# Optimization experiments

Measured on AMD Instinct MI355X. Metric: run time of the kernel, lower is better.

The kernel has to match this reference:

```python
import jax, jax.numpy as jnp
import numpy as np

B, T, HID = 2, 1024, 2048
NH, NKV, HD = 16, 4, 128
L, INTER = 4, 5632
EPS = 1e-6


def _rope_tables(key):
    inv_freq = 1.0 / (10000.0 ** (jnp.arange(0, HD, 2, dtype=jnp.float32) / HD))  # [HD/2]
    pos = jnp.arange(T, dtype=jnp.float32)
    freqs = pos[:, None] * inv_freq[None, :]          # [T, HD/2]
    emb = jnp.concatenate([freqs, freqs], axis=-1)    # [T, HD]
    cos = jnp.broadcast_to(jnp.cos(emb)[None], (B, T, HD))
    sin = jnp.broadcast_to(jnp.sin(emb)[None], (B, T, HD))
    return cos, sin


def setup_inputs() -> dict:
    key = jax.random.key(0)
    ks = jax.random.split(key, 12)
    std = 0.02
    cos, sin = _rope_tables(key)
    return {
        "hidden_states": jax.random.normal(ks[0], (B, T, HID), jnp.float32),
        "cos": cos,
        "sin": sin,
        "qw": jax.random.normal(ks[1], (L, NH * HD, HID), jnp.float32) * std,
        "qb": jnp.zeros((L, NH * HD), jnp.float32),
        "kw": jax.random.normal(ks[2], (L, NKV * HD, HID), jnp.float32) * std,
        "kb": jnp.zeros((L, NKV * HD), jnp.float32),
        "vw": jax.random.normal(ks[3], (L, NKV * HD, HID), jnp.float32) * std,
        "vb": jnp.zeros((L, NKV * HD), jnp.float32),
        "ow": jax.random.normal(ks[4], (L, HID, NH * HD), jnp.float32) * std,
        "gatew": jax.random.normal(ks[5], (L, INTER, HID), jnp.float32) * std,
        "upw": jax.random.normal(ks[6], (L, INTER, HID), jnp.float32) * std,
        "downw": jax.random.normal(ks[7], (L, HID, INTER), jnp.float32) * std,
        "ln1w": jnp.ones((L, HID), jnp.float32),
        "ln2w": jnp.ones((L, HID), jnp.float32),
        "normw": jnp.ones((HID,), jnp.float32),
    }


def _rmsnorm(x, w):
    xf = x.astype(jnp.float32)
    var = jnp.mean(xf * xf, axis=-1, keepdims=True)
    return (w * (xf * jax.lax.rsqrt(var + EPS))).astype(x.dtype)


def _rotate_half(x):
    x1, x2 = x[..., : HD // 2], x[..., HD // 2:]
    return jnp.concatenate([-x2, x1], axis=-1)


def _layer(x, cos, sin, mask, qw, qb, kw, kb, vw, vb, ow, gw, uw, dw, l1, l2):
    # --- attention (PreNorm) ---
    h = _rmsnorm(x, l1)
    q = (h @ qw.T + qb).reshape(B, T, NH, HD).transpose(0, 2, 1, 3)    # [B,NH,T,D]
    k = (h @ kw.T + kb).reshape(B, T, NKV, HD).transpose(0, 2, 1, 3)   # [B,NKV,T,D]
    v = (h @ vw.T + vb).reshape(B, T, NKV, HD).transpose(0, 2, 1, 3)
    c, s = cos[:, None], sin[:, None]                                  # [B,1,T,D]
    q = q * c + _rotate_half(q) * s
    k = k * c + _rotate_half(k) * s
    rep = NH // NKV
    k = jnp.repeat(k, rep, axis=1)                                     # GQA repeat_kv
    v = jnp.repeat(v, rep, axis=1)
    scores = jnp.einsum("bhqd,bhkd->bhqk", q, k) / (HD ** 0.5) + mask
    attn = jax.nn.softmax(scores.astype(jnp.float32), axis=-1).astype(q.dtype)
    ao = jnp.einsum("bhqk,bhkd->bhqd", attn, v)
    ao = ao.transpose(0, 2, 1, 3).reshape(B, T, NH * HD) @ ow.T
    x = x + ao
    # --- SwiGLU MLP (PreNorm) ---
    h = _rmsnorm(x, l2)
    x = x + (jax.nn.silu(h @ gw.T) * (h @ uw.T)) @ dw.T
    return x


def reference(hidden_states, cos, sin, qw, qb, kw, kb, vw, vb, ow,
              gatew, upw, downw, ln1w, ln2w, normw):
    min_val = jnp.finfo(hidden_states.dtype).min
    qpos = jnp.arange(T)
    mask = jnp.where(qpos[None, :] > qpos[:, None], min_val, 0.0).astype(hidden_states.dtype)
    mask = mask[None, None]  # [1,1,T,T]
    x = hidden_states
    for i in range(L):
        x = _layer(x, cos, sin, mask, qw[i], qb[i], kw[i], kb[i], vw[i], vb[i],
                   ow[i], gatew[i], upw[i], downw[i], ln1w[i], ln2w[i])
    return _rmsnorm(x, normw)
```

## Files before the change

kernel.cpp:

```cpp
#include <hip/hip_runtime.h>


typedef __attribute__((ext_vector_type(8))) __bf16 bf16x8;
typedef __attribute__((ext_vector_type(4))) float f32x4;
typedef __attribute__((ext_vector_type(4))) unsigned short u16x4;

#define DEV __device__ __forceinline__
#define BARRIER() asm volatile("s_barrier" ::: "memory")

#define NTOK 2048
#define HIDDIM 2048
#define KVDIM 512
#define HDIM 128
#define INTERDIM 5632

DEV unsigned short f2bf(float f) {
  union { float f; unsigned u; } a; a.f = f;
  unsigned r = a.u + 0x7fffu + ((a.u >> 16) & 1u);
  return (unsigned short)(r >> 16);
}
DEV float bf2f(unsigned short h) {
  union { unsigned u; float f; } a; a.u = ((unsigned)h) << 16;
  return a.f;
}
DEV unsigned short f2h(float f) {
  union { _Float16 h; unsigned short u; } c; c.h = (_Float16)f; return c.u;
}
DEV float h2f(unsigned short u) {
  union { unsigned short u; _Float16 h; } c; c.u = u; return (float)c.h;
}
DEV void gload_lds16(const void* g, void* l) {
  __builtin_amdgcn_global_load_lds(
      (const __attribute__((address_space(1))) unsigned int*)(g),
      (__attribute__((address_space(3))) unsigned int*)(l), 16, 0, 0);
}

__global__ __launch_bounds__(256) void cvt_kernel(
    const float* __restrict__ in, unsigned short* __restrict__ out, int n8) {
  const int i = blockIdx.x * 256 + threadIdx.x;
  if (i >= n8) return;
  const f32x4* p = reinterpret_cast<const f32x4*>(in) + (size_t)i * 2;
  const f32x4 a = p[0], b = p[1];
  bf16x8 o;
  o[0] = (__bf16)a.x; o[1] = (__bf16)a.y; o[2] = (__bf16)a.z; o[3] = (__bf16)a.w;
  o[4] = (__bf16)b.x; o[5] = (__bf16)b.y; o[6] = (__bf16)b.z; o[7] = (__bf16)b.w;
  *reinterpret_cast<bf16x8*>(out + (size_t)i * 8) = o;
}

__global__ __launch_bounds__(256) void cvt_gu(
    const float* __restrict__ gw, const float* __restrict__ uw,
    unsigned short* __restrict__ out) {
  const int i = blockIdx.x * 256 + threadIdx.x;
  const int row = i >> 8, g8 = i & 255;
  const int t = row >> 8, sub = row & 255;
  const float* src = (sub < 128)
                         ? gw + (size_t)(t * 128 + sub) * 2048
                         : uw + (size_t)(t * 128 + sub - 128) * 2048;
  const f32x4* p = reinterpret_cast<const f32x4*>(src) + (size_t)g8 * 2;
  const f32x4 a = p[0], b = p[1];
  bf16x8 o;
  o[0] = (__bf16)a.x; o[1] = (__bf16)a.y; o[2] = (__bf16)a.z; o[3] = (__bf16)a.w;
  o[4] = (__bf16)b.x; o[5] = (__bf16)b.y; o[6] = (__bf16)b.z; o[7] = (__bf16)b.w;
  *reinterpret_cast<bf16x8*>(out + (size_t)row * 2048 + g8 * 8) = o;
}

template <int OUTF32>
__global__ __launch_bounds__(256) void rmsnorm_kernel(
    const float* __restrict__ x, const float* __restrict__ w,
    void* __restrict__ outp) {
  const int row = blockIdx.x, tid = threadIdx.x;
  const int lane = tid & 63, wave = tid >> 6;
  const float* xr = x + (size_t)row * HIDDIM;
  f32x4 v0 = *reinterpret_cast<const f32x4*>(xr + tid * 4);
  f32x4 v1 = *reinterpret_cast<const f32x4*>(xr + 1024 + tid * 4);
  float ss = v0.x * v0.x + v0.y * v0.y + v0.z * v0.z + v0.w * v0.w +
             v1.x * v1.x + v1.y * v1.y + v1.z * v1.z + v1.w * v1.w;
#pragma unroll
  for (int off = 1; off < 64; off <<= 1) ss += __shfl_xor(ss, off, 64);
  __shared__ float red[4];
  if (lane == 0) red[wave] = ss;
  __syncthreads();
  ss = red[0] + red[1] + red[2] + red[3];
  const float rs = rsqrtf(ss * (1.0f / 2048.0f) + 1e-6f);
  f32x4 w0 = *reinterpret_cast<const f32x4*>(w + tid * 4);
  f32x4 w1 = *reinterpret_cast<const f32x4*>(w + 1024 + tid * 4);
  if (OUTF32) {
    float* o = (float*)outp + (size_t)row * HIDDIM;
    f32x4 o0, o1;
    o0.x = v0.x * rs * w0.x; o0.y = v0.y * rs * w0.y;
    o0.z = v0.z * rs * w0.z; o0.w = v0.w * rs * w0.w;
    o1.x = v1.x * rs * w1.x; o1.y = v1.y * rs * w1.y;
    o1.z = v1.z * rs * w1.z; o1.w = v1.w * rs * w1.w;
    *reinterpret_cast<f32x4*>(o + tid * 4) = o0;
    *reinterpret_cast<f32x4*>(o + 1024 + tid * 4) = o1;
  } else {
    unsigned short* o = (unsigned short*)outp + (size_t)row * HIDDIM;
    u16x4 p0, p1;
    p0.x = f2bf(v0.x * rs * w0.x); p0.y = f2bf(v0.y * rs * w0.y);
    p0.z = f2bf(v0.z * rs * w0.z); p0.w = f2bf(v0.w * rs * w0.w);
    p1.x = f2bf(v1.x * rs * w1.x); p1.y = f2bf(v1.y * rs * w1.y);
    p1.z = f2bf(v1.z * rs * w1.z); p1.w = f2bf(v1.w * rs * w1.w);
    *reinterpret_cast<u16x4*>(o + tid * 4) = p0;
    *reinterpret_cast<u16x4*>(o + 1024 + tid * 4) = p1;
  }
}

template <int KS, int OUTF32>
__global__ __launch_bounds__(256) void reduce_rms(
    float* __restrict__ x, const unsigned short* __restrict__ p, size_t zs,
    const float* __restrict__ w, void* __restrict__ outp) {
  const int row = blockIdx.x, tid = threadIdx.x;
  const int lane = tid & 63, wave = tid >> 6;
  float* xr = x + (size_t)row * HIDDIM;
  f32x4 v0 = *reinterpret_cast<const f32x4*>(xr + tid * 4);
  f32x4 v1 = *reinterpret_cast<const f32x4*>(xr + 1024 + tid * 4);
#pragma unroll
  for (int s = 0; s < KS; ++s) {
    const unsigned short* pr = p + (size_t)s * zs + (size_t)row * HIDDIM;
    u16x4 a = *reinterpret_cast<const u16x4*>(pr + tid * 4);
    u16x4 b = *reinterpret_cast<const u16x4*>(pr + 1024 + tid * 4);
    v0.x += bf2f(a.x); v0.y += bf2f(a.y); v0.z += bf2f(a.z); v0.w += bf2f(a.w);
    v1.x += bf2f(b.x); v1.y += bf2f(b.y); v1.z += bf2f(b.z); v1.w += bf2f(b.w);
  }
  *reinterpret_cast<f32x4*>(xr + tid * 4) = v0;
  *reinterpret_cast<f32x4*>(xr + 1024 + tid * 4) = v1;
  float ss = v0.x * v0.x + v0.y * v0.y + v0.z * v0.z + v0.w * v0.w +
             v1.x * v1.x + v1.y * v1.y + v1.z * v1.z + v1.w * v1.w;
#pragma unroll
  for (int off = 1; off < 64; off <<= 1) ss += __shfl_xor(ss, off, 64);
  __shared__ float red[4];
  if (lane == 0) red[wave] = ss;
  __syncthreads();
  ss = red[0] + red[1] + red[2] + red[3];
  const float rs = rsqrtf(ss * (1.0f / 2048.0f) + 1e-6f);
  f32x4 w0 = *reinterpret_cast<const f32x4*>(w + tid * 4);
  f32x4 w1 = *reinterpret_cast<const f32x4*>(w + 1024 + tid * 4);
  if (OUTF32) {
    float* o = (float*)outp + (size_t)row * HIDDIM;
    f32x4 o0, o1;
    o0.x = v0.x * rs * w0.x; o0.y = v0.y * rs * w0.y;
    o0.z = v0.z * rs * w0.z; o0.w = v0.w * rs * w0.w;
    o1.x = v1.x * rs * w1.x; o1.y = v1.y * rs * w1.y;
    o1.z = v1.z * rs * w1.z; o1.w = v1.w * rs * w1.w;
    *reinterpret_cast<f32x4*>(o + tid * 4) = o0;
    *reinterpret_cast<f32x4*>(o + 1024 + tid * 4) = o1;
  } else {
    unsigned short* o = (unsigned short*)outp + (size_t)row * HIDDIM;
    u16x4 p0, p1;
    p0.x = f2bf(v0.x * rs * w0.x); p0.y = f2bf(v0.y * rs * w0.y);
    p0.z = f2bf(v0.z * rs * w0.z); p0.w = f2bf(v0.w * rs * w0.w);
    p1.x = f2bf(v1.x * rs * w1.x); p1.y = f2bf(v1.y * rs * w1.y);
    p1.z = f2bf(v1.z * rs * w1.z); p1.w = f2bf(v1.w * rs * w1.w);
    *reinterpret_cast<u16x4*>(o + tid * 4) = p0;
    *reinterpret_cast<u16x4*>(o + 1024 + tid * 4) = p1;
  }
}

struct G16Setup {
  const unsigned short* srcp0;
  const unsigned short* srcp1;
  int ldsc0, ldsc1;
};

DEV G16Setup g16_setup(const unsigned short* A, const unsigned short* W,
                       int K, int m0, int n0, int t0, int wave, int lane) {
  const int c0 = wave * 2, c1 = wave * 2 + 1;
  const int rA = lane >> 2, cg = (lane & 3) * 8;
  G16Setup s;
  const unsigned short* gb[4] = {
      A + (size_t)m0 * K, A + (size_t)(m0 + 128) * K,
      W + (size_t)n0 * K, W + (size_t)(n0 + 128) * K};
  s.srcp0 = gb[c0 >> 3] + (size_t)((c0 & 7) * 16 + rA) * K + cg +
            (size_t)t0 * 32;
  s.srcp1 = gb[c1 >> 3] + (size_t)((c1 & 7) * 16 + rA) * K + cg +
            (size_t)t0 * 32;
  s.ldsc0 = c0 * 512;
  s.ldsc1 = c1 * 512;
  return s;
}

#define G16STAGE(st_, tt_, c_)                                                \
  do {                                                                        \
    gload_lds16(st_.srcp0 + (size_t)(tt_)*32, &lds[(c_)*16384 + st_.ldsc0]);  \
    gload_lds16(st_.srcp1 + (size_t)(tt_)*32, &lds[(c_)*16384 + st_.ldsc1]);  \
  } while (0)

#define G16LDA(mi_, c_)                                                       \
  (*reinterpret_cast<const bf16x8*>(                                          \
      &lds[(c_)*16384 + (wm >> 1) * 4096 +                                    \
           (((wm & 1) * 64) + (mi_)*16 + fr) * 32 + lq * 8]))
#define G16LDB(ni_, c_)                                                       \
  (*reinterpret_cast<const bf16x8*>(                                          \
      &lds[(c_)*16384 + (2 + (wn >> 1)) * 4096 +                              \
           (((wn & 1) * 64) + (ni_)*16 + fr) * 32 + lq * 8]))

#define G16KLOOP(NT_)                                                         \
  G16STAGE(st, 0, 0);                                                         \
  for (int t = 0; t < (NT_); ++t) {                                           \
    const int c = t & 1;                                                      \
    if (t + 1 < (NT_)) {                                                      \
      G16STAGE(st, t + 1, c ^ 1);                                             \
      asm volatile("s_waitcnt vmcnt(2)" ::: "memory");                        \
    } else {                                                                  \
      asm volatile("s_waitcnt vmcnt(0)" ::: "memory");                        \
    }                                                                         \
    BARRIER();                                                                \
    bf16x8 aF[4], bF[4];                                                      \
    bF[0] = G16LDB(0, c); bF[1] = G16LDB(1, c);                               \
    bF[2] = G16LDB(2, c); bF[3] = G16LDB(3, c);                               \
    aF[0] = G16LDA(0, c); aF[1] = G16LDA(1, c);                               \
    aF[2] = G16LDA(2, c); aF[3] = G16LDA(3, c);                               \
    __builtin_amdgcn_s_setprio(1);                                            \
    _Pragma("unroll") for (int ni = 0; ni < 4; ++ni)                          \
        _Pragma("unroll") for (int mi = 0; mi < 4; ++mi)                      \
            acc[mi][ni] = __builtin_amdgcn_mfma_f32_16x16x32_bf16(            \
                aF[mi], bF[ni], acc[mi][ni], 0, 0, 0);                        \
    __builtin_amdgcn_s_setprio(0);                                            \
    __builtin_amdgcn_sched_barrier(0);                                        \
    BARRIER();                                                                \
  }

__global__ __launch_bounds__(1024) void gemm16w(
    const unsigned short* __restrict__ A, const unsigned short* __restrict__ W,
    unsigned short* __restrict__ outp, int K, int ldo, int kt_split,
    int kt_tot, size_t zstride) {
  __shared__ unsigned short lds[32768];
  const int tid = threadIdx.x, lane = tid & 63, wave = tid >> 6;
  const int fr = lane & 15, lq = lane >> 4;
  const int wm = wave >> 2, wn = wave & 3;

  int bx = blockIdx.x, by = blockIdx.y;
  {
    const int nbx = gridDim.x, nwg = nbx * gridDim.y;
    const int lin = by * nbx + bx, cpx = nwg >> 3;
    const int swz = (lin & 7) * cpx + (lin >> 3);
    bx = swz % nbx; by = swz / nbx;
  }
  const int m0 = by * 256, n0 = bx * 256;
  const int bz = blockIdx.z;
  const int t0 = bz * kt_split;
  int NT = kt_tot - t0; if (NT > kt_split) NT = kt_split;

  G16Setup st = g16_setup(A, W, K, m0, n0, t0, wave, lane);
  f32x4 acc[4][4] = {};
  G16KLOOP(NT);

  const int r0 = lq * 4;
#pragma unroll
  for (int mi = 0; mi < 4; ++mi)
#pragma unroll
    for (int ni = 0; ni < 4; ++ni)
#pragma unroll
      for (int r = 0; r < 4; ++r) {
        const int gm = m0 + wm * 64 + mi * 16 + r0 + r;
        const int gn = n0 + wn * 64 + ni * 16 + fr;
        outp[(size_t)bz * zstride + (size_t)gm * ldo + gn] =
            f2bf(acc[mi][ni][r]);
      }
}

__global__ __launch_bounds__(1024) void gemm_gu16(
    const unsigned short* __restrict__ A, const unsigned short* __restrict__ W,
    unsigned short* __restrict__ act) {
  __shared__ unsigned short lds[32768];
  const int tid = threadIdx.x, lane = tid & 63, wave = tid >> 6;
  const int fr = lane & 15, lq = lane >> 4;
  const int wm = wave >> 2, wn = wave & 3;
  const int K = 2048;

  int bx = blockIdx.x, by = blockIdx.y;
  {
    const int nbx = gridDim.x, nwg = nbx * gridDim.y;
    const int lin = by * nbx + bx, cpx = nwg >> 3;
    const int swz = (lin & 7) * cpx + (lin >> 3);
    bx = swz % nbx; by = swz / nbx;
  }
  const int m0 = by * 256, n0 = bx * 256;

  G16Setup st = g16_setup(A, W, K, m0, n0, 0, wave, lane);
  f32x4 acc[4][4] = {};
  G16KLOOP(64);

  float* fl = reinterpret_cast<float*>(lds);
  const int r0 = lq * 4;
#pragma unroll 1
  for (int rd = 0; rd < 4; ++rd) {
    __syncthreads();
    if (wm == rd && wn < 2) {
#pragma unroll
      for (int mi = 0; mi < 4; ++mi)
#pragma unroll
        for (int ni = 0; ni < 4; ++ni)
#pragma unroll
          for (int r = 0; r < 4; ++r)
            fl[(mi * 16 + r0 + r) * 128 + wn * 64 + ni * 16 + fr] =
                acc[mi][ni][r];
    }
    __syncthreads();
    if (wm == rd && wn >= 2) {
      const int wnu = wn - 2;
#pragma unroll
      for (int mi = 0; mi < 4; ++mi)
#pragma unroll
        for (int ni = 0; ni < 4; ++ni)
#pragma unroll
          for (int r = 0; r < 4; ++r) {
            const int mrow = mi * 16 + r0 + r;
            const float g = fl[mrow * 128 + wnu * 64 + ni * 16 + fr];
            const float s = g / (1.f + __expf(-g));
            const int gm = m0 + wm * 64 + mrow;
            const int ic = (n0 >> 1) + wnu * 64 + ni * 16 + fr;
            act[(size_t)gm * INTERDIM + ic] = f2bf(s * acc[mi][ni][r]);
          }
    }
  }
}

template <int MB>
DEV void mfma16(const bf16x8 (&aF)[4], const bf16x8 (&bF)[4],
                f32x4 (&acc)[8][4]) {
#pragma unroll
  for (int ni = 0; ni < 4; ++ni)
#pragma unroll
    for (int mi = 0; mi < 4; ++mi)
      acc[MB + mi][ni] = __builtin_amdgcn_mfma_f32_16x16x32_bf16(
          aF[mi], bF[ni], acc[MB + mi][ni], 0, 0, 0);
}

__global__ __launch_bounds__(512, 2) void gemm_qk(
    const unsigned short* __restrict__ q, const unsigned short* __restrict__ k,
    unsigned short* __restrict__ s) {
  __shared__ unsigned short lds[65536];
  const int tid = threadIdx.x, lane = tid & 63, wave = tid >> 6;
  const int fr = lane & 15, lq = lane >> 4;
  const int wm = wave >> 2, wn = wave & 3;

  int bx = blockIdx.x, by = blockIdx.y;
  {
    const int nbx = gridDim.x, nwg = nbx * gridDim.y;
    const int lin = by * nbx + bx, cpx = nwg >> 3;
    const int swz = (lin & 7) * cpx + (lin >> 3);
    bx = swz % nbx; by = swz / nbx;
  }
  if (bx > by) return;
  const int z = blockIdx.z, b = z >> 4, h = z & 15, kvh = h >> 2;
  const unsigned short* A = q + (size_t)b * 1024 * HIDDIM + h * HDIM;
  const unsigned short* W = k + (size_t)b * 1024 * KVDIM + kvh * HDIM;
  unsigned short* outp = s + (size_t)z * 1048576;
  const int m0 = by * 256, n0 = bx * 256;

  const int u0 = tid, u1 = tid + 512;
  const int r0s = u0 >> 3, r1s = u1 >> 3;
  const int c0 = ((u0 & 7) ^ (r0s & 7)) << 3, c1 = ((u1 & 7) ^ (r1s & 7)) << 3;
  const size_t offA0 = (size_t)r0s * HIDDIM + c0;
  const size_t offA1 = (size_t)r1s * HIDDIM + c1;
  const size_t offW0 = (size_t)r0s * KVDIM + c0;
  const size_t offW1 = (size_t)r1s * KVDIM + c1;
  const unsigned short* gb0 = A + (size_t)m0 * HIDDIM;
  const unsigned short* gb1 = A + (size_t)(m0 + 128) * HIDDIM;
  const unsigned short* gb2 = W + (size_t)n0 * KVDIM;
  const unsigned short* gb3 = W + (size_t)(n0 + 128) * KVDIM;

#define QSTAGE(h_, tt_, b_)                                                   \
  do {                                                                        \
    const unsigned short* _g =                                                \
        ((h_) == 0 ? gb0 : (h_) == 1 ? gb1 : (h_) == 2 ? gb2 : gb3) +         \
        (size_t)(tt_)*64;                                                     \
    const size_t _o0 = (h_) < 2 ? offA0 : offW0;                              \
    const size_t _o1 = (h_) < 2 ? offA1 : offW1;                              \
    unsigned short* _l = &lds[(b_)*32768 + (h_)*8192 + wave * 512];           \
    gload_lds16(_g + _o0, _l);                                                \
    gload_lds16(_g + _o1, _l + 4096);                                         \
  } while (0)

  const int e0 = lq ^ (fr & 7);
  const int cbA = wm * 8192;
  const int cbB = (2 + (wn >> 1)) * 8192;
  const int rB0 = (wn & 1) * 64 + fr;

#define QLDA(mi_, ks_, c_)                                                    \
  (*reinterpret_cast<const bf16x8*>(                                          \
      &lds[(c_)*32768 + cbA + ((mi_)*16 + fr) * 64 + ((e0 ^ ((ks_)*4)) << 3)]))
#define QLDB(ni_, ks_, c_)                                                    \
  (*reinterpret_cast<const bf16x8*>(                                          \
      &lds[(c_)*32768 + cbB + (rB0 + (ni_)*16) * 64 + ((e0 ^ ((ks_)*4)) << 3)]))

  f32x4 acc[8][4] = {};
  bf16x8 aF[4], bF[4];

  QSTAGE(0, 0, 0); QSTAGE(1, 0, 0); QSTAGE(2, 0, 0); QSTAGE(3, 0, 0);

  for (int t = 0; t < 2; ++t) {
    const int c = t & 1;
    if (t == 0) {
      QSTAGE(0, 1, 1); QSTAGE(2, 1, 1);
      asm volatile("s_waitcnt vmcnt(4)" ::: "memory");
    } else {
      asm volatile("s_waitcnt vmcnt(0)" ::: "memory");
    }
    BARRIER();
    bF[0] = QLDB(0, 0, c); bF[1] = QLDB(1, 0, c);
    bF[2] = QLDB(2, 0, c); bF[3] = QLDB(3, 0, c);
    aF[0] = QLDA(0, 0, c); aF[1] = QLDA(1, 0, c);
    aF[2] = QLDA(2, 0, c); aF[3] = QLDA(3, 0, c);
    if (t == 0) { QSTAGE(1, 1, 1); QSTAGE(3, 1, 1); }
    BARRIER();
    __builtin_amdgcn_s_setprio(1);
    mfma16<0>(aF, bF, acc);
    __builtin_amdgcn_s_setprio(0);
    __builtin_amdgcn_sched_barrier(0);
    BARRIER();
    aF[0] = QLDA(4, 0, c); aF[1] = QLDA(5, 0, c);
    aF[2] = QLDA(6, 0, c); aF[3] = QLDA(7, 0, c);
    BARRIER();
    __builtin_amdgcn_s_setprio(1);
    mfma16<4>(aF, bF, acc);
    __builtin_amdgcn_s_setprio(0);
    __builtin_amdgcn_sched_barrier(0);
    BARRIER();
    bF[0] = QLDB(0, 1, c); bF[1] = QLDB(1, 1, c);
    bF[2] = QLDB(2, 1, c); bF[3] = QLDB(3, 1, c);
    aF[0] = QLDA(0, 1, c); aF[1] = QLDA(1, 1, c);
    aF[2] = QLDA(2, 1, c); aF[3] = QLDA(3, 1, c);
    BARRIER();
    __builtin_amdgcn_s_setprio(1);
    mfma16<0>(aF, bF, acc);
    __builtin_amdgcn_s_setprio(0);
    __builtin_amdgcn_sched_barrier(0);
    BARRIER();
    aF[0] = QLDA(4, 1, c); aF[1] = QLDA(5, 1, c);
    aF[2] = QLDA(6, 1, c); aF[3] = QLDA(7, 1, c);
    BARRIER();
    __builtin_amdgcn_s_setprio(1);
    mfma16<4>(aF, bF, acc);
    __builtin_amdgcn_s_setprio(0);
    __builtin_amdgcn_sched_barrier(0);
    BARRIER();
  }

  const float scale = 0.08838834764831845f;
  const int r0 = lq * 4;
#pragma unroll
  for (int mi = 0; mi < 8; ++mi)
#pragma unroll
    for (int ni = 0; ni < 4; ++ni)
#pragma unroll
      for (int r = 0; r < 4; ++r) {
        const int gm = m0 + wm * 128 + mi * 16 + r0 + r;
        const int gn = n0 + wn * 64 + ni * 16 + fr;
        outp[(size_t)gm * 1024 + gn] = f2h(acc[mi][ni][r] * scale);
      }
#undef QSTAGE
#undef QLDA
#undef QLDB
}

__global__ __launch_bounds__(256) void softmax_rows(unsigned short* __restrict__ s) {
  const int row = blockIdx.x, tid = threadIdx.x;
  const int lane = tid & 63, wave = tid >> 6;
  const int qv = row & 1023;
  const int nact = ((qv >> 8) + 1) << 8;
  unsigned short* r = s + (size_t)row * 1024;
  const int col = tid * 4;
  const bool act = (col < nact);
  float v[4];
  if (act) {
    u16x4 raw = *reinterpret_cast<const u16x4*>(r + col);
#pragma unroll
    for (int j = 0; j < 4; ++j)
      v[j] = (col + j <= qv) ? h2f(((unsigned short*)&raw)[j]) : -1e30f;
  } else {
#pragma unroll
    for (int j = 0; j < 4; ++j) v[j] = -1e30f;
  }
  float mx = fmaxf(fmaxf(v[0], v[1]), fmaxf(v[2], v[3]));
#pragma unroll
  for (int off = 1; off < 64; off <<= 1) mx = fmaxf(mx, __shfl_xor(mx, off, 64));
  __shared__ float redm[4], reds[4];
  if (lane == 0) redm[wave] = mx;
  __syncthreads();
  const float M = fmaxf(fmaxf(redm[0], redm[1]), fmaxf(redm[2], redm[3]));
  float e[4], ts = 0.f;
#pragma unroll
  for (int j = 0; j < 4; ++j) {
    e[j] = (act && col + j <= qv) ? __expf(v[j] - M) : 0.f;
    ts += e[j];
  }
#pragma unroll
  for (int off = 1; off < 64; off <<= 1) ts += __shfl_xor(ts, off, 64);
  if (lane == 0) reds[wave] = ts;
  __syncthreads();
  const float inv = 1.f / (reds[0] + reds[1] + reds[2] + reds[3]);
  if (act) {
    u16x4 o;
    o.x = f2bf(e[0] * inv); o.y = f2bf(e[1] * inv);
    o.z = f2bf(e[2] * inv); o.w = f2bf(e[3] * inv);
    *reinterpret_cast<u16x4*>(r + col) = o;
  }
}

__global__ __launch_bounds__(256, 2) void gemm_pv(
    const unsigned short* __restrict__ p, const unsigned short* __restrict__ vt,
    unsigned short* __restrict__ ao) {
  __shared__ unsigned short lds[40960];
  const int tid = threadIdx.x, lane = tid & 63, wave = tid >> 6;
  const int fr = lane & 15, lq = lane >> 4;
  const int bxn = blockIdx.x, by = blockIdx.y, z = blockIdx.z;
  const int b = z >> 4, h = z & 15, kvh = h >> 2;
  const int m0p = by * 256, n0 = bxn * 64;
  const int NT = by * 4 + 4;

  const unsigned short* A = p + (size_t)z * 1048576 + (size_t)m0p * 1024;
  const unsigned short* W =
      vt + ((size_t)(b * 4 + kvh) * 128 + n0) * 1024;

#define PVSTAGE(tt_, c_)                                                      \
  do {                                                                        \
    _Pragma("unroll")                                                         \
    for (int j = 0; j < 8; ++j) {                                             \
      const int u = wave * 512 + j * 64 + lane;                               \
      const int rw = u >> 3;                                                  \
      gload_lds16(A + (size_t)rw * 1024 + (((u & 7) ^ (rw & 7)) << 3) +       \
                      (size_t)(tt_)*64,                                       \
                  &lds[(c_)*20480 + wave * 4096 + j * 512]);                  \
    }                                                                         \
    _Pragma("unroll")                                                         \
    for (int j = 0; j < 2; ++j) {                                             \
      const int u = wave * 128 + j * 64 + lane;                               \
      const int rw = u >> 3;                                                  \
      gload_lds16(W + (size_t)rw * 1024 + (((u & 7) ^ (rw & 7)) << 3) +       \
                      (size_t)(tt_)*64,                                       \
                  &lds[(c_)*20480 + 16384 + wave * 1024 + j * 512]);          \
    }                                                                         \
  } while (0)

  const int e0 = lq ^ (fr & 7);
#define PVLDA(mi_, ks_, c_)                                                   \
  (*reinterpret_cast<const bf16x8*>(                                          \
      &lds[(c_)*20480 + (wave * 64 + (mi_)*16 + fr) * 64 +                    \
           ((e0 ^ ((ks_)*4)) << 3)]))
#define PVLDB(ni_, ks_, c_)                                                   \
  (*reinterpret_cast<const bf16x8*>(                                          \
      &lds[(c_)*20480 + 16384 + ((ni_)*16 + fr) * 64 +                        \
           ((e0 ^ ((ks_)*4)) << 3)]))

  f32x4 acc[4][4] = {};
  bf16x8 aF[4], bF[4];

  PVSTAGE(0, 0);

  for (int t = 0; t < NT; ++t) {
    const int c = t & 1;
    if (t + 1 < NT) {
      PVSTAGE(t + 1, c ^ 1);
      asm volatile("s_waitcnt vmcnt(10)" ::: "memory");
    } else {
      asm volatile("s_waitcnt vmcnt(0)" ::: "memory");
    }
    BARRIER();
#pragma unroll
    for (int ks = 0; ks < 2; ++ks) {
      bF[0] = PVLDB(0, ks, c); bF[1] = PVLDB(1, ks, c);
      bF[2] = PVLDB(2, ks, c); bF[3] = PVLDB(3, ks, c);
      aF[0] = PVLDA(0, ks, c); aF[1] = PVLDA(1, ks, c);
      aF[2] = PVLDA(2, ks, c); aF[3] = PVLDA(3, ks, c);
      BARRIER();
      __builtin_amdgcn_s_setprio(1);
#pragma unroll
      for (int ni = 0; ni < 4; ++ni)
#pragma unroll
        for (int mi = 0; mi < 4; ++mi)
          acc[mi][ni] = __builtin_amdgcn_mfma_f32_16x16x32_bf16(
              aF[mi], bF[ni], acc[mi][ni], 0, 0, 0);
      __builtin_amdgcn_s_setprio(0);
      __builtin_amdgcn_sched_barrier(0);
      BARRIER();
    }
  }

  const int r0 = lq * 4;
#pragma unroll
  for (int mi = 0; mi < 4; ++mi)
#pragma unroll
    for (int ni = 0; ni < 4; ++ni)
#pragma unroll
      for (int r = 0; r < 4; ++r) {
        const int gm = m0p + wave * 64 + mi * 16 + r0 + r;
        const int gn = n0 + ni * 16 + fr;
        ao[(size_t)(b * 1024 + gm) * HIDDIM + h * HDIM + gn] =
            f2bf(acc[mi][ni][r]);
      }
#undef PVSTAGE
#undef PVLDA
#undef PVLDB
}

__global__ __launch_bounds__(256) void reduce_qkv(
    const unsigned short* __restrict__ p, const float* __restrict__ qb,
    const float* __restrict__ kb, const float* __restrict__ vb,
    const float* __restrict__ cosb, const float* __restrict__ sinb,
    unsigned short* __restrict__ qo, unsigned short* __restrict__ ko,
    unsigned short* __restrict__ vto) {
  const int i = blockIdx.x * 256 + threadIdx.x;
  const int row = i / 768, c4 = (i - row * 768) * 4;
  const unsigned short* p0 = p + (size_t)row * 3072;
  const unsigned short* p1 = p + 6291456 + (size_t)row * 3072;
  const u16x4 a0 = *reinterpret_cast<const u16x4*>(p0 + c4);
  const u16x4 a1 = *reinterpret_cast<const u16x4*>(p1 + c4);
  f32x4 s;
  s.x = bf2f(a0.x) + bf2f(a1.x); s.y = bf2f(a0.y) + bf2f(a1.y);
  s.z = bf2f(a0.z) + bf2f(a1.z); s.w = bf2f(a0.w) + bf2f(a1.w);
  if (c4 < 2560) {
    const float* bias; unsigned short* out; int d, ldo;
    if (c4 < 2048) { bias = qb; out = qo; d = c4;        ldo = HIDDIM; }
    else           { bias = kb; out = ko; d = c4 - 2048; ldo = KVDIM; }
    const int dd = d & 127;
    const bool lohalf = (dd < 64);
    const int pc = lohalf ? c4 + 64 : c4 - 64;
    const int pd = lohalf ? d + 64 : d - 64;
    const u16x4 b0 = *reinterpret_cast<const u16x4*>(p0 + pc);
    const u16x4 b1 = *reinterpret_cast<const u16x4*>(p1 + pc);
    f32x4 sp;
    sp.x = bf2f(b0.x) + bf2f(b1.x); sp.y = bf2f(b0.y) + bf2f(b1.y);
    sp.z = bf2f(b0.z) + bf2f(b1.z); sp.w = bf2f(b0.w) + bf2f(b1.w);
    const f32x4 bv = *reinterpret_cast<const f32x4*>(bias + d);
    const f32x4 bp = *reinterpret_cast<const f32x4*>(bias + pd);
    const f32x4 cv = *reinterpret_cast<const f32x4*>(cosb + (size_t)row * 128 + dd);
    const f32x4 sv = *reinterpret_cast<const f32x4*>(sinb + (size_t)row * 128 + dd);
    const f32x4 xv = s + bv, pv = sp + bp;
    f32x4 o;
    if (lohalf) o = xv * cv - pv * sv;
    else        o = xv * cv + pv * sv;
    u16x4 ob;
    ob.x = f2bf(o.x); ob.y = f2bf(o.y); ob.z = f2bf(o.z); ob.w = f2bf(o.w);
    *reinterpret_cast<u16x4*>(out + (size_t)row * ldo + d) = ob;
  } else {
    const int d = c4 - 2560;
    const int kvh = d >> 7, dd = d & 127;
    const int b = row >> 10, t = row & 1023;
    const f32x4 bv = *reinterpret_cast<const f32x4*>(vb + d);
    const f32x4 o = s + bv;
    unsigned short* vr =
        vto + ((size_t)(b * 4 + kvh) * 128 + dd) * 1024 + t;
    vr[0] = f2bf(o.x); vr[1024] = f2bf(o.y);
    vr[2048] = f2bf(o.z); vr[3072] = f2bf(o.w);
  }
}

extern "C" void kernel_launch(void* const* d_in, const int* in_sizes, int n_in,
                              void* d_out, int out_size, void* d_ws,
                              size_t ws_size, hipStream_t stream) {
  (void)in_sizes; (void)n_in; (void)out_size; (void)ws_size;
  const float* hidden = (const float*)d_in[0];
  const float* cosb  = (const float*)d_in[1];
  const float* sinb  = (const float*)d_in[2];
  const float* qw    = (const float*)d_in[3];
  const float* qbias = (const float*)d_in[4];
  const float* kw    = (const float*)d_in[5];
  const float* kbias = (const float*)d_in[6];
  const float* vw    = (const float*)d_in[7];
  const float* vbias = (const float*)d_in[8];
  const float* ow    = (const float*)d_in[9];
  const float* gw    = (const float*)d_in[10];
  const float* uw    = (const float*)d_in[11];
  const float* dw    = (const float*)d_in[12];
  const float* ln1   = (const float*)d_in[13];
  const float* ln2   = (const float*)d_in[14];
  const float* normw = (const float*)d_in[15];

  char* ws = (char*)d_ws;
  float* x               = (float*)ws;
  unsigned short* hbuf   = (unsigned short*)(ws + 16777216);
  unsigned short* qbuf   = (unsigned short*)(ws + 25165824);
  unsigned short* kbuf   = (unsigned short*)(ws + 33554432);
  unsigned short* vtbuf  = (unsigned short*)(ws + 35651584);
  unsigned short* aobuf  = (unsigned short*)(ws + 39845888);
  unsigned short* actbuf = (unsigned short*)(ws + 71303168);
  unsigned short* wcvt   = (unsigned short*)(ws + 94371840);
  unsigned short* pbQKV = (unsigned short*)(ws + 37748736);
  unsigned short* sbuf  = (unsigned short*)(ws + 48234496);
  unsigned short* pbO   = (unsigned short*)(ws + 48234496);
  unsigned short* wgu   = (unsigned short*)(ws + 25165824);
  unsigned short* pbD   = (unsigned short*)(ws + 25165824);

  unsigned short* wq16 = wcvt;
  unsigned short* wk16 = wcvt + 4194304;
  unsigned short* wv16 = wcvt + 5242880;
  unsigned short* ow16 = wcvt;

  hipMemcpyAsync(x, hidden, (size_t)NTOK * HIDDIM * 4,
                 hipMemcpyDeviceToDevice, stream);
  rmsnorm_kernel<0><<<NTOK, 256, 0, stream>>>(x, ln1, hbuf);

  for (int l = 0; l < 4; ++l) {
    const float* qw_l = qw + (size_t)l * 2048 * 2048;
    const float* qb_l = qbias + (size_t)l * 2048;
    const float* kw_l = kw + (size_t)l * 512 * 2048;
    const float* kb_l = kbias + (size_t)l * 512;
    const float* vw_l = vw + (size_t)l * 512 * 2048;
    const float* vb_l = vbias + (size_t)l * 512;
    const float* ow_l = ow + (size_t)l * 2048 * 2048;
    const float* gw_l = gw + (size_t)l * 5632 * 2048;
    const float* uw_l = uw + (size_t)l * 5632 * 2048;
    const float* dw_l = dw + (size_t)l * 2048 * 5632;

    cvt_kernel<<<2048, 256, 0, stream>>>(qw_l, wq16, 524288);
    cvt_kernel<<<512, 256, 0, stream>>>(kw_l, wk16, 131072);
    cvt_kernel<<<512, 256, 0, stream>>>(vw_l, wv16, 131072);
    gemm16w<<<dim3(12, 8, 2), 1024, 0, stream>>>(
        hbuf, wcvt, pbQKV, 2048, 3072, 32, 64, (size_t)6291456);
    reduce_qkv<<<6144, 256, 0, stream>>>(pbQKV, qb_l, kb_l, vb_l, cosb, sinb,
                                         qbuf, kbuf, vtbuf);

    gemm_qk<<<dim3(4, 4, 32), 512, 0, stream>>>(qbuf, kbuf, sbuf);
    softmax_rows<<<32768, 256, 0, stream>>>(sbuf);
    gemm_pv<<<dim3(2, 4, 32), 256, 0, stream>>>(sbuf, vtbuf, aobuf);

    cvt_kernel<<<2048, 256, 0, stream>>>(ow_l, ow16, 524288);
    gemm16w<<<dim3(8, 8, 4), 1024, 0, stream>>>(
        aobuf, ow16, pbO, 2048, 2048, 16, 64, (size_t)4194304);
    reduce_rms<4, 0><<<NTOK, 256, 0, stream>>>(x, pbO, (size_t)4194304,
                                               ln2 + l * 2048, hbuf);

    cvt_gu<<<11264, 256, 0, stream>>>(gw_l, uw_l, wgu);
    gemm_gu16<<<dim3(44, 8), 1024, 0, stream>>>(hbuf, wgu, actbuf);

    cvt_kernel<<<5632, 256, 0, stream>>>(dw_l, wcvt, 1441792);
    gemm16w<<<dim3(8, 8, 4), 1024, 0, stream>>>(
        actbuf, wcvt, pbD, 5632, 2048, 44, 176, (size_t)4194304);
    if (l < 3) {
      reduce_rms<4, 0><<<NTOK, 256, 0, stream>>>(
          x, pbD, (size_t)4194304, ln1 + (l + 1) * 2048, hbuf);
    } else {
      reduce_rms<4, 1><<<NTOK, 256, 0, stream>>>(x, pbD, (size_t)4194304,
                                                 normw, d_out);
    }
  }
}
```

Baseline: 1.710 ms.

## Rework projection GEMMs to 8 waves with 4-stage LDS pipeline and XOR swizzle

Swaps the 16-wave, double-buffered 256x256 GEMM kernels for an 8-wave version. Each wave now computes a 128x64 sub-tile with twice the accumulators. The K loop moves to a 4-deep LDS ring with 3 stages prefetched, and LDS rows use an XOR swizzle to cut bank conflicts on fragment reads. Two blocks per CU are requested via launch bounds, and the gate/up SiLU epilogue is simplified to a single LDS exchange round. In exchange there is more register pressure from the doubled accumulators, 128KB of LDS per block, and extra barriers that split each K step into two MFMA halves.

Result: no change. 1.705 ms (-0.3%).

```diff
diff --git a/kernel.cpp b/kernel.cpp
--- a/kernel.cpp
+++ b/kernel.cpp
@@ -156,75 +156,100 @@
   }
 }
 
-struct G16Setup {
-  const unsigned short* srcp0;
-  const unsigned short* srcp1;
-  int ldsc0, ldsc1;
+template <int MB>
+DEV void mfma16(const bf16x8 (&aF)[4], const bf16x8 (&bF)[4],
+                f32x4 (&acc)[8][4]) {
+#pragma unroll
+  for (int ni = 0; ni < 4; ++ni)
+#pragma unroll
+    for (int mi = 0; mi < 4; ++mi)
+      acc[MB + mi][ni] = __builtin_amdgcn_mfma_f32_16x16x32_bf16(
+          aF[mi], bF[ni], acc[MB + mi][ni], 0, 0, 0);
+}
+
+struct G8D {
+  const unsigned short* src[4];
+  int dstbase[4];
 };
 
-DEV G16Setup g16_setup(const unsigned short* A, const unsigned short* W,
-                       int K, int m0, int n0, int t0, int wave, int lane) {
-  const int c0 = wave * 2, c1 = wave * 2 + 1;
-  const int rA = lane >> 2, cg = (lane & 3) * 8;
-  G16Setup s;
-  const unsigned short* gb[4] = {
-      A + (size_t)m0 * K, A + (size_t)(m0 + 128) * K,
-      W + (size_t)n0 * K, W + (size_t)(n0 + 128) * K};
-  s.srcp0 = gb[c0 >> 3] + (size_t)((c0 & 7) * 16 + rA) * K + cg +
-            (size_t)t0 * 32;
-  s.srcp1 = gb[c1 >> 3] + (size_t)((c1 & 7) * 16 + rA) * K + cg +
-            (size_t)t0 * 32;
-  s.ldsc0 = c0 * 512;
-  s.ldsc1 = c1 * 512;
-  return s;
-}
-
-#define G16STAGE(st_, tt_, c_)                                                \
+DEV G8D g8d_setup(const unsigned short* A, const unsigned short* W, int K,
+                  int m0, int n0, int t0, int wave, int lane) {
+  G8D g;
+  const int rl = lane >> 2;
+  const int sl = ((lane & 3) ^ ((lane >> 3) & 3)) * 8;
+#pragma unroll
+  for (int j = 0; j < 4; ++j) {
+    const int q0 = wave * 256 + j * 64;
+    const int s = q0 >> 9;
+    const int r0 = (q0 & 511) >> 2;
+    const unsigned short* mat =
+        (s < 2) ? A + (size_t)(m0 + s * 128) * K
+                : W + (size_t)(n0 + (s - 2) * 128) * K;
+    g.src[j] = mat + (size_t)(r0 + rl) * K + sl + (size_t)t0 * 32;
+    g.dstbase[j] = q0 * 8;
+  }
+  return g;
+}
+
+#define G8DSTAGE(g_, t_, c_)                                                  \
   do {                                                                        \
-    gload_lds16(st_.srcp0 + (size_t)(tt_)*32, &lds[(c_)*16384 + st_.ldsc0]);  \
-    gload_lds16(st_.srcp1 + (size_t)(tt_)*32, &lds[(c_)*16384 + st_.ldsc1]);  \
+    _Pragma("unroll") for (int j = 0; j < 4; ++j)                             \
+        gload_lds16(g_.src[j] + (size_t)(t_)*32,                              \
+                    &lds[(c_)*16384 + g_.dstbase[j]]);                        \
   } while (0)
 
-#define G16LDA(mi_, c_)                                                       \
+#define D8LDA(mi_, c_)                                                        \
   (*reinterpret_cast<const bf16x8*>(                                          \
-      &lds[(c_)*16384 + (wm >> 1) * 4096 +                                    \
-           (((wm & 1) * 64) + (mi_)*16 + fr) * 32 + lq * 8]))
-#define G16LDB(ni_, c_)                                                       \
+      &lds[(c_)*16384 + wm * 4096 + ((mi_)*16 + fr) * 32 +                    \
+           (lq ^ ((fr >> 1) & 3)) * 8]))
+#define D8LDB(ni_, c_)                                                        \
   (*reinterpret_cast<const bf16x8*>(                                          \
       &lds[(c_)*16384 + (2 + (wn >> 1)) * 4096 +                              \
-           (((wn & 1) * 64) + (ni_)*16 + fr) * 32 + lq * 8]))
-
-#define G16KLOOP(NT_)                                                         \
-  G16STAGE(st, 0, 0);                                                         \
-  for (int t = 0; t < (NT_); ++t) {                                           \
-    const int c = t & 1;                                                      \
-    if (t + 1 < (NT_)) {                                                      \
-      G16STAGE(st, t + 1, c ^ 1);                                             \
-      asm volatile("s_waitcnt vmcnt(2)" ::: "memory");                        \
-    } else {                                                                  \
+           ((wn & 1) * 64 + (ni_)*16 + fr) * 32 +                             \
+           (lq ^ ((fr >> 1) & 3)) * 8]))
+
+#define D8KLOOP(NS_)                                                          \
+  if ((NS_) > 0) G8DSTAGE(g, 0, 0);                                           \
+  if ((NS_) > 1) G8DSTAGE(g, 1, 1);                                           \
+  if ((NS_) > 2) G8DSTAGE(g, 2, 2);                                           \
+  for (int t = 0; t < (NS_); ++t) {                                           \
+    const int c = t & 3;                                                      \
+    if (t + 3 < (NS_)) G8DSTAGE(g, t + 3, (t + 3) & 3);                       \
+    const int rem = (NS_)-1 - t;                                              \
+    if (rem >= 3)                                                             \
+      asm volatile("s_waitcnt vmcnt(12)" ::: "memory");                       \
+    else if (rem == 2)                                                        \
+      asm volatile("s_waitcnt vmcnt(8)" ::: "memory");                        \
+    else if (rem == 1)                                                        \
+      asm volatile("s_waitcnt vmcnt(4)" ::: "memory");                        \
+    else                                                                      \
       asm volatile("s_waitcnt vmcnt(0)" ::: "memory");                        \
-    }                                                                         \
     BARRIER();                                                                \
-    bf16x8 aF[4], bF[4];                                                      \
-    bF[0] = G16LDB(0, c); bF[1] = G16LDB(1, c);                               \
-    bF[2] = G16LDB(2, c); bF[3] = G16LDB(3, c);                               \
-    aF[0] = G16LDA(0, c); aF[1] = G16LDA(1, c);                               \
-    aF[2] = G16LDA(2, c); aF[3] = G16LDA(3, c);                               \
+    bF[0] = D8LDB(0, c); bF[1] = D8LDB(1, c);                                 \
+    bF[2] = D8LDB(2, c); bF[3] = D8LDB(3, c);                                 \
+    aF[0] = D8LDA(0, c); aF[1] = D8LDA(1, c);                                 \
+    aF[2] = D8LDA(2, c); aF[3] = D8LDA(3, c);                                 \
+    BARRIER();                                                                \
     __builtin_amdgcn_s_setprio(1);                                            \
-    _Pragma("unroll") for (int ni = 0; ni < 4; ++ni)                          \
-        _Pragma("unroll") for (int mi = 0; mi < 4; ++mi)                      \
-            acc[mi][ni] = __builtin_amdgcn_mfma_f32_16x16x32_bf16(            \
-                aF[mi], bF[ni], acc[mi][ni], 0, 0, 0);                        \
+    mfma16<0>(aF, bF, acc);                                                   \
     __builtin_amdgcn_s_setprio(0);                                            \
     __builtin_amdgcn_sched_barrier(0);                                        \
     BARRIER();                                                                \
-  }
-
-__global__ __launch_bounds__(1024) void gemm16w(
+    aF[0] = D8LDA(4, c); aF[1] = D8LDA(5, c);                                 \
+    aF[2] = D8LDA(6, c); aF[3] = D8LDA(7, c);                                 \
+    BARRIER();                                                                \
+    __builtin_amdgcn_s_setprio(1);                                            \
+    mfma16<4>(aF, bF, acc);                                                   \
+    __builtin_amdgcn_s_setprio(0);                                            \
+    __builtin_amdgcn_sched_barrier(0);                                        \
+    BARRIER();                                                                \
+  }
+
+__global__ __launch_bounds__(512, 2) void gemm8d(
     const unsigned short* __restrict__ A, const unsigned short* __restrict__ W,
     unsigned short* __restrict__ outp, int K, int ldo, int kt_split,
     int kt_tot, size_t zstride) {
-  __shared__ unsigned short lds[32768];
+  __shared__ unsigned short lds[65536];
   const int tid = threadIdx.x, lane = tid & 63, wave = tid >> 6;
   const int fr = lane & 15, lq = lane >> 4;
   const int wm = wave >> 2, wn = wave & 3;
@@ -239,30 +264,31 @@
   const int m0 = by * 256, n0 = bx * 256;
   const int bz = blockIdx.z;
   const int t0 = bz * kt_split;
-  int NT = kt_tot - t0; if (NT > kt_split) NT = kt_split;
-
-  G16Setup st = g16_setup(A, W, K, m0, n0, t0, wave, lane);
-  f32x4 acc[4][4] = {};
-  G16KLOOP(NT);
+  int NS = kt_tot - t0; if (NS > kt_split) NS = kt_split;
+
+  G8D g = g8d_setup(A, W, K, m0, n0, t0, wave, lane);
+  f32x4 acc[8][4] = {};
+  bf16x8 aF[4], bF[4];
+  D8KLOOP(NS);
 
   const int r0 = lq * 4;
 #pragma unroll
-  for (int mi = 0; mi < 4; ++mi)
+  for (int mi = 0; mi < 8; ++mi)
 #pragma unroll
     for (int ni = 0; ni < 4; ++ni)
 #pragma unroll
       for (int r = 0; r < 4; ++r) {
-        const int gm = m0 + wm * 64 + mi * 16 + r0 + r;
+        const int gm = m0 + wm * 128 + mi * 16 + r0 + r;
         const int gn = n0 + wn * 64 + ni * 16 + fr;
         outp[(size_t)bz * zstride + (size_t)gm * ldo + gn] =
             f2bf(acc[mi][ni][r]);
       }
 }
 
-__global__ __launch_bounds__(1024) void gemm_gu16(
+__global__ __launch_bounds__(512, 2) void gemm_gu8d(
     const unsigned short* __restrict__ A, const unsigned short* __restrict__ W,
     unsigned short* __restrict__ act) {
-  __shared__ unsigned short lds[32768];
+  __shared__ unsigned short lds[65536];
   const int tid = threadIdx.x, lane = tid & 63, wave = tid >> 6;
   const int fr = lane & 15, lq = lane >> 4;
   const int wm = wave >> 2, wn = wave & 3;
@@ -277,54 +303,41 @@
   }
   const int m0 = by * 256, n0 = bx * 256;
 
-  G16Setup st = g16_setup(A, W, K, m0, n0, 0, wave, lane);
-  f32x4 acc[4][4] = {};
-  G16KLOOP(64);
+  G8D g = g8d_setup(A, W, K, m0, n0, 0, wave, lane);
+  f32x4 acc[8][4] = {};
+  bf16x8 aF[4], bF[4];
+  D8KLOOP(64);
 
   float* fl = reinterpret_cast<float*>(lds);
   const int r0 = lq * 4;
-#pragma unroll 1
-  for (int rd = 0; rd < 4; ++rd) {
-    __syncthreads();
-    if (wm == rd && wn < 2) {
-#pragma unroll
-      for (int mi = 0; mi < 4; ++mi)
-#pragma unroll
-        for (int ni = 0; ni < 4; ++ni)
-#pragma unroll
-          for (int r = 0; r < 4; ++r)
-            fl[(mi * 16 + r0 + r) * 128 + wn * 64 + ni * 16 + fr] =
-                acc[mi][ni][r];
-    }
-    __syncthreads();
-    if (wm == rd && wn >= 2) {
-      const int wnu = wn - 2;
-#pragma unroll
-      for (int mi = 0; mi < 4; ++mi)
-#pragma unroll
-        for (int ni = 0; ni < 4; ++ni)
-#pragma unroll
-          for (int r = 0; r < 4; ++r) {
-            const int mrow = mi * 16 + r0 + r;
-            const float g = fl[mrow * 128 + wnu * 64 + ni * 16 + fr];
-            const float s = g / (1.f + __expf(-g));
-            const int gm = m0 + wm * 64 + mrow;
-            const int ic = (n0 >> 1) + wnu * 64 + ni * 16 + fr;
-            act[(size_t)gm * INTERDIM + ic] = f2bf(s * acc[mi][ni][r]);
-          }
-    }
-  }
-}
-
-template <int MB>
-DEV void mfma16(const bf16x8 (&aF)[4], const bf16x8 (&bF)[4],
-                f32x4 (&acc)[8][4]) {
-#pragma unroll
-  for (int ni = 0; ni < 4; ++ni)
-#pragma unroll
-    for (int mi = 0; mi < 4; ++mi)
-      acc[MB + mi][ni] = __builtin_amdgcn_mfma_f32_16x16x32_bf16(
-          aF[mi], bF[ni], acc[MB + mi][ni], 0, 0, 0);
+  __syncthreads();
+  if (wn < 2) {
+#pragma unroll
+    for (int mi = 0; mi < 8; ++mi)
+#pragma unroll
+      for (int ni = 0; ni < 4; ++ni)
+#pragma unroll
+        for (int r = 0; r < 4; ++r)
+          fl[wm * 16384 + (mi * 16 + r0 + r) * 128 + wn * 64 + ni * 16 + fr] =
+              acc[mi][ni][r];
+  }
+  __syncthreads();
+  if (wn >= 2) {
+    const int wnu = wn - 2;
+#pragma unroll
+    for (int mi = 0; mi < 8; ++mi)
+#pragma unroll
+      for (int ni = 0; ni < 4; ++ni)
+#pragma unroll
+        for (int r = 0; r < 4; ++r) {
+          const int mrow = mi * 16 + r0 + r;
+          const float gv = fl[wm * 16384 + mrow * 128 + wnu * 64 + ni * 16 + fr];
+          const float s = gv / (1.f + __expf(-gv));
+          const int gm = m0 + wm * 128 + mrow;
+          const int ic = (n0 >> 1) + wnu * 64 + ni * 16 + fr;
+          act[(size_t)gm * INTERDIM + ic] = f2bf(s * acc[mi][ni][r]);
+        }
+  }
 }
 
 __global__ __launch_bounds__(512, 2) void gemm_qk(
@@ -707,7 +720,7 @@
     cvt_kernel<<<2048, 256, 0, stream>>>(qw_l, wq16, 524288);
     cvt_kernel<<<512, 256, 0, stream>>>(kw_l, wk16, 131072);
     cvt_kernel<<<512, 256, 0, stream>>>(vw_l, wv16, 131072);
-    gemm16w<<<dim3(12, 8, 2), 1024, 0, stream>>>(
+    gemm8d<<<dim3(12, 8, 2), 512, 0, stream>>>(
         hbuf, wcvt, pbQKV, 2048, 3072, 32, 64, (size_t)6291456);
     reduce_qkv<<<6144, 256, 0, stream>>>(pbQKV, qb_l, kb_l, vb_l, cosb, sinb,
                                          qbuf, kbuf, vtbuf);
@@ -717,16 +730,16 @@
     gemm_pv<<<dim3(2, 4, 32), 256, 0, stream>>>(sbuf, vtbuf, aobuf);
 
     cvt_kernel<<<2048, 256, 0, stream>>>(ow_l, ow16, 524288);
-    gemm16w<<<dim3(8, 8, 4), 1024, 0, stream>>>(
+    gemm8d<<<dim3(8, 8, 4), 512, 0, stream>>>(
         aobuf, ow16, pbO, 2048, 2048, 16, 64, (size_t)4194304);
     reduce_rms<4, 0><<<NTOK, 256, 0, stream>>>(x, pbO, (size_t)4194304,
                                                ln2 + l * 2048, hbuf);
 
     cvt_gu<<<11264, 256, 0, stream>>>(gw_l, uw_l, wgu);
-    gemm_gu16<<<dim3(44, 8), 1024, 0, stream>>>(hbuf, wgu, actbuf);
+    gemm_gu8d<<<dim3(44, 8), 512, 0, stream>>>(hbuf, wgu, actbuf);
 
     cvt_kernel<<<5632, 256, 0, stream>>>(dw_l, wcvt, 1441792);
-    gemm16w<<<dim3(8, 8, 4), 1024, 0, stream>>>(
+    gemm8d<<<dim3(8, 8, 4), 512, 0, stream>>>(
         actbuf, wcvt, pbD, 5632, 2048, 44, 176, (size_t)4194304);
     if (l < 3) {
       reduce_rms<4, 0><<<NTOK, 256, 0, stream>>>(
```
